# Kernel tuning notes

Measured on AMD Instinct MI355X. Metric: run time of the kernel, lower is better.

The kernel has to match this reference:

```python
import jax, jax.numpy as jnp
import numpy as np

MASK_FILL = jnp.float32(-2**32 + 1)

def dice(x, alpha):
    # x: (S, B, F); batch-dim (dim=0) mean/std, unbiased std like torch.std
    avg = x.mean(axis=0)
    std = jnp.std(x, axis=0, ddof=1)
    p = jax.nn.sigmoid((x - avg) / std)
    return x * p + alpha * x * (1.0 - p)

def setup_inputs() -> dict:
    key = jax.random.key(0)
    ks = jax.random.split(key, 12)
    S, B, D = 200, 1024, 128          # seq_len, batch, 2H
    F = 4 * D                          # num_features = 512
    L1, L2 = 80, 40
    inp = {
        "query": jax.random.normal(ks[0], (B, D), jnp.float32),
        "facts": jax.random.normal(ks[1], (S, B, D), jnp.float32),
        "mask": jax.random.randint(ks[2], (S, B), 0, 2).astype(bool),
        "W1": jax.random.normal(ks[3], (F, L1), jnp.float32) / np.sqrt(F),
        "b1": jnp.zeros((L1,), jnp.float32),
        "a1": jnp.zeros((1,), jnp.float32),
        "W2": jax.random.normal(ks[4], (L1, L2), jnp.float32) / np.sqrt(L1),
        "b2": jnp.zeros((L2,), jnp.float32),
        "a2": jnp.zeros((1,), jnp.float32),
        "W3": jax.random.normal(ks[5], (L2, 1), jnp.float32) / np.sqrt(L2),
        "b3": jnp.zeros((1,), jnp.float32),
    }
    return inp

def reference(query, facts, mask, W1, b1, a1, W2, b2, a2, W3, b3):
    S, B, D = facts.shape
    # faithful to torch: tile along feature dim then reshape (permutes elements)
    q2 = jnp.tile(query, (1, S)).reshape(S, B, D)
    x = jnp.concatenate([q2, facts, q2 * facts, q2 - facts], axis=-1)  # (S,B,4D)
    h = dice(jnp.einsum('sbf,fl->sbl', x, W1) + b1, a1)
    h = dice(jnp.einsum('sbf,fl->sbl', h, W2) + b2, a2)
    logits = (jnp.einsum('sbf,fl->sbl', h, W3) + b3).squeeze(-1)  # (S,B)
    masked = jnp.where(mask, logits, MASK_FILL)
    normalized = jax.nn.softmax(masked, axis=0)
    return normalized[..., None] * facts  # (S,B,D)
```

## Files before the change

kernel.cpp:

```cpp
#include <hip/hip_runtime.h>
#include <hip/hip_bf16.h>
#include <math.h>

#define SS 200
#define BB 1024
#define DD 128
#define FF 512
#define LL1 80
#define LL2 40
#define PP (SS*BB)
#define MASK_FILL_F (-4294967295.0f)
#define NTILE 13

typedef short bf16x8 __attribute__((ext_vector_type(8)));
typedef float f32x4  __attribute__((ext_vector_type(4)));

static __device__ __forceinline__ unsigned short f2bf(float x) {
    __hip_bfloat16 h = __float2bfloat16(x);
    return *reinterpret_cast<unsigned short*>(&h);
}
static __device__ __forceinline__ float bf2f(unsigned short u) {
    __hip_bfloat16 h = *reinterpret_cast<__hip_bfloat16*>(&u);
    return __bfloat162float(h);
}
static __device__ __forceinline__ void split8(const float* x, bf16x8& ah, bf16x8& al) {
#pragma unroll
    for (int j = 0; j < 8; ++j) {
        unsigned u = __float_as_uint(x[j]);
        ah[j] = (short)(u >> 16);
        float hi = __uint_as_float(u & 0xffff0000u);
        al[j] = (short)f2bf(x[j] - hi);
    }
}
static __device__ __forceinline__ float fast_sigmoid(float t) {
    return __builtin_amdgcn_rcpf(1.f + __expf(-t));
}

__global__ void k_prep_all(const float* __restrict__ W1, const float* __restrict__ W2,
                           const unsigned char* __restrict__ mask,
                           unsigned short* __restrict__ bfr1,
                           unsigned short* __restrict__ bfr2, int* __restrict__ flag) {
    const int blk = blockIdx.x;
    if (blk == 35) {
        if (threadIdx.x < 64) {
            const uchar4 u = ((const uchar4*)mask)[threadIdx.x];
            const bool f = ((u.y | u.z) | u.w) != 0;
            const unsigned long long anyf = __ballot(f);
            if (threadIdx.x == 0) *flag = (anyf != 0ull) ? 1 : 0;
        }
        return;
    }
    if (blk < 30) {
        int t = blk * 256 + threadIdx.x;
        if (t >= 120 * 64) return;
        int lane = t & 63;
        int fid  = t >> 6;
        int nt   = fid % 5;
        int hl   = (fid / 5) % 2;
        int step = (fid / 10) % 6;
        int h    = fid / 60;
        int ktL  = step / 3;
        int seg  = step - 3 * ktL;
        int kt   = h * 2 + ktL;
        int n     = nt * 16 + (lane & 15);
        int kbase = kt * 32 + (lane >> 4) * 8;
        unsigned short* o = bfr1 + (size_t)t * 8;
#pragma unroll
        for (int j = 0; j < 8; ++j) {
            int k = kbase + j;
            float w;
            if (seg == 0)      w = W1[k * LL1 + n] + W1[(384 + k) * LL1 + n];
            else if (seg == 1) w = W1[(128 + k) * LL1 + n] - W1[(384 + k) * LL1 + n];
            else               w = W1[(256 + k) * LL1 + n];
            unsigned short hb = f2bf(w);
            o[j] = (hl == 0) ? hb : f2bf(w - bf2f(hb));
        }
    } else {
        int t = (blk - 30) * 256 + threadIdx.x;
        if (t >= 18 * 64) return;
        int lane = t & 63;
        int fid  = t >> 6;
        int hl   = fid & 1;
        int nt   = (fid >> 1) % 3;
        int kt   = fid / 6;
        int n  = nt * 16 + (lane & 15);
        int kb = kt * 32 + (lane >> 4) * 8;
        unsigned short* o = bfr2 + (size_t)t * 8;
#pragma unroll
        for (int j = 0; j < 8; ++j) {
            int k = kb + j;
            float w = (k < LL1 && n < LL2) ? W2[k * LL2 + n] : 0.f;
            unsigned short hb = f2bf(w);
            o[j] = (hl == 0) ? hb : f2bf(w - bf2f(hb));
        }
    }
}

__global__ __launch_bounds__(512, 4) void k_fused(
    const float* __restrict__ query, const float* __restrict__ facts,
    const unsigned short* __restrict__ bfr1, const unsigned short* __restrict__ bfr2,
    const float* __restrict__ b1, const float* __restrict__ a1,
    const float* __restrict__ b2, const float* __restrict__ a2,
    const float* __restrict__ W3, const float* __restrict__ b3,
    const void* __restrict__ mask, const int* __restrict__ flag,
    float* __restrict__ wbufT) {
    const int tid  = threadIdx.x;
    const int w    = tid >> 6;
    const int lane = tid & 63;
    const int m    = lane & 15;
    const int quad = lane >> 4;
    const int b    = blockIdx.x;

    __shared__ __align__(16) float z1f[NTILE * 16 * 81 + 16];
    __shared__ float psum[480], pssq[480];
    __shared__ float smean[LL1], sistd[LL1];
    __shared__ float sw3[LL2];
    __shared__ float red[8];

    int tile[2], pr[2], qr[2];
    bool tl[2];
#pragma unroll
    for (int t = 0; t < 2; ++t) {
        tile[t] = t * 8 + w;
        tl[t]   = (tile[t] < NTILE);
        int s = tile[t] * 16 + m;
        if (s > SS - 1) s = SS - 1;
        pr[t] = s * BB + b;
        qr[t] = pr[t] / SS;
    }

    f32x4 acc[2][5];
#pragma unroll
    for (int t = 0; t < 2; ++t)
#pragma unroll
        for (int nt = 0; nt < 5; ++nt) acc[t][nt] = (f32x4){0.f, 0.f, 0.f, 0.f};

#pragma unroll 1
    for (int h = 0; h < 2; ++h) {
        if (h) __syncthreads();
        {
            const int4* src = (const int4*)bfr1 + h * 3840;
            int4* dst = (int4*)z1f;
#pragma unroll
            for (int it = 0; it < 8; ++it) {
                int idx = it * 512 + tid;
                if (idx < 3840) dst[idx] = src[idx];
            }
        }
        __syncthreads();
        const unsigned short* lbuf = (const unsigned short*)z1f;
#pragma unroll
        for (int ktL = 0; ktL < 2; ++ktL) {
            const int dbase = (h * 2 + ktL) * 32 + quad * 8;
            float q8[2][8], f8[2][8];
#pragma unroll
            for (int t = 0; t < 2; ++t) {
                if (!tl[t]) continue;
                const float* qp = query + (size_t)qr[t] * DD + dbase;
                const float* fp = facts + (size_t)pr[t] * DD + dbase;
                *(float4*)&q8[t][0] = *(const float4*)qp;
                *(float4*)&q8[t][4] = *(const float4*)(qp + 4);
                *(float4*)&f8[t][0] = *(const float4*)fp;
                *(float4*)&f8[t][4] = *(const float4*)(fp + 4);
            }
#pragma unroll
            for (int seg = 0; seg < 3; ++seg) {
                const int step = ktL * 3 + seg;
                bf16x8 Bh[5], Bl[5];
#pragma unroll
                for (int nt = 0; nt < 5; ++nt) {
                    Bh[nt] = *(const bf16x8*)&lbuf[((step * 2 + 0) * 5 + nt) * 512 + lane * 8];
                    Bl[nt] = *(const bf16x8*)&lbuf[((step * 2 + 1) * 5 + nt) * 512 + lane * 8];
                }
#pragma unroll
                for (int t = 0; t < 2; ++t) {
                    if (!tl[t]) continue;
                    float x8[8];
#pragma unroll
                    for (int j = 0; j < 8; ++j)
                        x8[j] = (seg == 0) ? q8[t][j]
                              : (seg == 1 ? f8[t][j] : q8[t][j] * f8[t][j]);
                    bf16x8 ah, al;
                    split8(x8, ah, al);
#pragma unroll
                    for (int nt = 0; nt < 5; ++nt) {
                        acc[t][nt] = __builtin_amdgcn_mfma_f32_16x16x32_bf16(ah, Bh[nt], acc[t][nt], 0, 0, 0);
                        acc[t][nt] = __builtin_amdgcn_mfma_f32_16x16x32_bf16(al, Bh[nt], acc[t][nt], 0, 0, 0);
                        acc[t][nt] = __builtin_amdgcn_mfma_f32_16x16x32_bf16(ah, Bl[nt], acc[t][nt], 0, 0, 0);
                    }
                }
            }
        }
    }

    __syncthreads();
    {
        float b1v[5];
#pragma unroll
        for (int nt = 0; nt < 5; ++nt) b1v[nt] = b1[nt * 16 + m];
#pragma unroll
        for (int t = 0; t < 2; ++t) {
            if (!tl[t]) continue;
#pragma unroll
            for (int nt = 0; nt < 5; ++nt)
#pragma unroll
                for (int r = 0; r < 4; ++r)
                    z1f[(tile[t] * 16 + quad * 4 + r) * 81 + nt * 16 + m] = acc[t][nt][r] + b1v[nt];
        }
    }
    __syncthreads();

    if (tid < 480) {
        const int l = tid % LL1, c = tid / LL1;
        const int s0 = c * 34;
        const int s1 = (s0 + 34 < SS) ? s0 + 34 : SS;
        float sum = 0.f, ssq = 0.f;
        for (int s = s0; s < s1; ++s) {
            float v = z1f[s * 81 + l];
            sum += v;
            ssq = fmaf(v, v, ssq);
        }
        psum[c * LL1 + l] = sum;
        pssq[c * LL1 + l] = ssq;
    }
    __syncthreads();
    if (tid < LL1) {
        float sum = 0.f, ssq = 0.f;
#pragma unroll
        for (int c = 0; c < 6; ++c) {
            sum += psum[c * LL1 + tid];
            ssq += pssq[c * LL1 + tid];
        }
        float mn  = sum * (1.f / SS);
        float var = (ssq - (float)SS * mn * mn) * (1.f / (SS - 1));
        smean[tid] = mn;
        sistd[tid] = rsqrtf(var);
    }
    __syncthreads();

    const float alpha1 = *a1;
    f32x4 acc2[2][3];
#pragma unroll
    for (int t = 0; t < 2; ++t)
#pragma unroll
        for (int nt = 0; nt < 3; ++nt) acc2[t][nt] = (f32x4){0.f, 0.f, 0.f, 0.f};

#pragma unroll
    for (int kt = 0; kt < 3; ++kt) {
        bf16x8 Bh[3], Bl[3];
#pragma unroll
        for (int nt = 0; nt < 3; ++nt) {
            Bh[nt] = *(const bf16x8*)(bfr2 + (size_t)((kt * 3 + nt) * 2 + 0) * 512 + lane * 8);
            Bl[nt] = *(const bf16x8*)(bfr2 + (size_t)((kt * 3 + nt) * 2 + 1) * 512 + lane * 8);
        }
        const int kb = kt * 32 + quad * 8;
        const bool lv = (kt < 2 || quad < 2);
#pragma unroll
        for (int t = 0; t < 2; ++t) {
            if (!tl[t]) continue;
            float x8[8];
            if (lv) {
                const float* zr = &z1f[(tile[t] * 16 + m) * 81 + kb];
#pragma unroll
                for (int j = 0; j < 8; ++j) {
                    float v  = zr[j];
                    float pp = fast_sigmoid((v - smean[kb + j]) * sistd[kb + j]);
                    x8[j] = v * (alpha1 + (1.f - alpha1) * pp);
                }
            } else {
#pragma unroll
                for (int j = 0; j < 8; ++j) x8[j] = 0.f;
            }
            bf16x8 ah, al;
            split8(x8, ah, al);
#pragma unroll
            for (int nt = 0; nt < 3; ++nt) {
                acc2[t][nt] = __builtin_amdgcn_mfma_f32_16x16x32_bf16(ah, Bh[nt], acc2[t][nt], 0, 0, 0);
                acc2[t][nt] = __builtin_amdgcn_mfma_f32_16x16x32_bf16(al, Bh[nt], acc2[t][nt], 0, 0, 0);
                acc2[t][nt] = __builtin_amdgcn_mfma_f32_16x16x32_bf16(ah, Bl[nt], acc2[t][nt], 0, 0, 0);
            }
        }
    }
    __syncthreads();

    {
        float b2v[3];
#pragma unroll
        for (int nt = 0; nt < 3; ++nt) {
            const int n = nt * 16 + m;
            b2v[nt] = (n < LL2) ? b2[n] : 0.f;
        }
#pragma unroll
        for (int t = 0; t < 2; ++t) {
            if (!tl[t]) continue;
#pragma unroll
            for (int r = 0; r < 4; ++r) {
                const int srow = tile[t] * 16 + quad * 4 + r;
                if (srow >= SS) continue;
#pragma unroll
                for (int nt = 0; nt < 3; ++nt) {
                    const int n = nt * 16 + m;
                    if (n < LL2) z1f[srow * 41 + n] = acc2[t][nt][r] + b2v[nt];
                }
            }
        }
    }
    __syncthreads();

    if (tid < 480) {
        const int l = tid % LL2, c = tid / LL2;
        const int s0 = c * 17;
        const int s1 = (s0 + 17 < SS) ? s0 + 17 : SS;
        float sum = 0.f, ssq = 0.f;
        for (int s = s0; s < s1; ++s) {
            float v = z1f[s * 41 + l];
            sum += v;
            ssq = fmaf(v, v, ssq);
        }
        psum[c * LL2 + l] = sum;
        pssq[c * LL2 + l] = ssq;
    }
    __syncthreads();
    if (tid < LL2) {
        float sum = 0.f, ssq = 0.f;
#pragma unroll
        for (int c = 0; c < 12; ++c) {
            sum += psum[c * LL2 + tid];
            ssq += pssq[c * LL2 + tid];
        }
        float mn  = sum * (1.f / SS);
        float var = (ssq - (float)SS * mn * mn) * (1.f / (SS - 1));
        smean[tid] = mn;
        sistd[tid] = rsqrtf(var);
        sw3[tid]   = W3[tid];
    }
    __syncthreads();

    const float alpha2 = *a2;
    const int boolLayout = *flag;
    float logit = -3.0e38f;
    if (tid < SS) {
        float dot = b3[0];
#pragma unroll
        for (int k = 0; k < LL2; ++k) {
            float v  = z1f[tid * 41 + k];
            float pp = fast_sigmoid((v - smean[k]) * sistd[k]);
            float hh = v * (pp + alpha2 * (1.f - pp));
            dot = fmaf(hh, sw3[k], dot);
        }
        const int mi = tid * BB + b;
        const bool mk = boolLayout ? (((const unsigned char*)mask)[mi] != 0)
                                   : (((const int*)mask)[mi] != 0);
        logit = mk ? dot : MASK_FILL_F;
    }
    float v = logit;
#pragma unroll
    for (int off = 1; off < 64; off <<= 1) v = fmaxf(v, __shfl_xor(v, off, 64));
    if ((tid & 63) == 0) red[tid >> 6] = v;
    __syncthreads();
    float smax = red[0];
#pragma unroll
    for (int i = 1; i < 8; ++i) smax = fmaxf(smax, red[i]);
    __syncthreads();
    const float e = (tid < SS) ? __expf(logit - smax) : 0.f;
    v = e;
#pragma unroll
    for (int off = 1; off < 64; off <<= 1) v += __shfl_xor(v, off, 64);
    if ((tid & 63) == 0) red[tid >> 6] = v;
    __syncthreads();
    float ssum = red[0];
#pragma unroll
    for (int i = 1; i < 8; ++i) ssum += red[i];
    const float inv = __builtin_amdgcn_rcpf(ssum);
    if (tid < SS) wbufT[(size_t)b * SS + tid] = e * inv;
}

__global__ __launch_bounds__(256) void k4_scale(
    const float* __restrict__ wbufT, const float* __restrict__ facts,
    float* __restrict__ out) {
    int i = blockIdx.x * 256 + threadIdx.x;
    int p = i >> 5;
    float w = wbufT[(size_t)(p & (BB - 1)) * SS + (p >> 10)];
    float4 f = ((const float4*)facts)[i];
    float4 o;
    o.x = f.x * w; o.y = f.y * w; o.z = f.z * w; o.w = f.w * w;
    ((float4*)out)[i] = o;
}

extern "C" void kernel_launch(void* const* d_in, const int* in_sizes, int n_in,
                              void* d_out, int out_size, void* d_ws, size_t ws_size,
                              hipStream_t stream) {
    const float* query = (const float*)d_in[0];
    const float* facts = (const float*)d_in[1];
    const void*  mask  = d_in[2];
    const float* W1 = (const float*)d_in[3];
    const float* b1 = (const float*)d_in[4];
    const float* a1 = (const float*)d_in[5];
    const float* W2 = (const float*)d_in[6];
    const float* b2 = (const float*)d_in[7];
    const float* a2 = (const float*)d_in[8];
    const float* W3 = (const float*)d_in[9];
    const float* b3 = (const float*)d_in[10];
    float* out = (float*)d_out;

    unsigned short* bfr1 = (unsigned short*)(out + 24739840);
    unsigned short* bfr2 = (unsigned short*)(out + 24801280);
    float* wbufT = (float*)d_ws;
    int*   flag  = (int*)((char*)d_ws + 900 * 1024);

    k_prep_all<<<36, 256, 0, stream>>>(W1, W2, (const unsigned char*)mask, bfr1, bfr2, flag);
    k_fused<<<BB, 512, 0, stream>>>(query, facts, bfr1, bfr2, b1, a1, b2, a2,
                                    W3, b3, mask, flag, wbufT);
    k4_scale<<<(PP * DD) / (256 * 4), 256, 0, stream>>>(wbufT, facts, out);
}
```

Baseline: 328.9 us.

## Split fused kernel into a coalesced MFMA layer-1 kernel and per-batch reduction kernel

The fused per-batch kernel loaded facts and query rows strided across the sequence dimension, one batch column per block. The first-layer MFMA GEMM now runs in its own kernel over contiguous position tiles, giving coalesced facts reads and more blocks. It writes the pre-activation z1 transposed, in batch-major order, into the output buffer as scratch. A second kernel then reloads each batch's z1 slab for the Dice statistics, layer 2 and the softmax. This adds a round trip of about 65 MB through global memory plus an extra launch.

```diff
diff --git a/kernel.cpp b/kernel.cpp
--- a/kernel.cpp
+++ b/kernel.cpp
@@ -96,14 +96,103 @@
     }
 }
 
-__global__ __launch_bounds__(512, 4) void k_fused(
+__global__ __launch_bounds__(256, 4) void k1_mfma(
     const float* __restrict__ query, const float* __restrict__ facts,
-    const unsigned short* __restrict__ bfr1, const unsigned short* __restrict__ bfr2,
-    const float* __restrict__ b1, const float* __restrict__ a1,
-    const float* __restrict__ b2, const float* __restrict__ a2,
-    const float* __restrict__ W3, const float* __restrict__ b3,
-    const void* __restrict__ mask, const int* __restrict__ flag,
-    float* __restrict__ wbufT) {
+    const unsigned short* __restrict__ bfr, const float* __restrict__ b1,
+    float* __restrict__ z1T) {
+    const int tid  = threadIdx.x;
+    const int lane = tid & 63;
+    const int m    = lane & 15;
+    const int quad = lane >> 4;
+    const int pw   = blockIdx.x * 128 + (tid >> 6) * 32;
+
+    __shared__ __align__(16) unsigned short lbuf[15360];
+
+    f32x4 acc[2][5];
+#pragma unroll
+    for (int t = 0; t < 2; ++t)
+#pragma unroll
+        for (int nt = 0; nt < 5; ++nt) acc[t][nt] = (f32x4){0.f, 0.f, 0.f, 0.f};
+
+    int pr[2], qr[2];
+#pragma unroll
+    for (int t = 0; t < 2; ++t) {
+        pr[t] = pw + t * 16 + m;
+        qr[t] = pr[t] / SS;
+    }
+
+#pragma unroll 1
+    for (int kt = 0; kt < 4; ++kt) {
+        const int dbase = kt * 32 + quad * 8;
+        float q8[2][8], f8[2][8];
+#pragma unroll
+        for (int t = 0; t < 2; ++t) {
+            const float* qp = query + (size_t)qr[t] * DD + dbase;
+            const float* fp = facts + (size_t)pr[t] * DD + dbase;
+            *(float4*)&q8[t][0] = *(const float4*)qp;
+            *(float4*)&q8[t][4] = *(const float4*)(qp + 4);
+            *(float4*)&f8[t][0] = *(const float4*)fp;
+            *(float4*)&f8[t][4] = *(const float4*)(fp + 4);
+        }
+        if (kt) __syncthreads();
+        {
+            const int4* src = (const int4*)bfr + kt * 1920;
+#pragma unroll
+            for (int it = 0; it < 8; ++it) {
+                int idx = it * 256 + tid;
+                if (idx < 1920) ((int4*)lbuf)[idx] = src[idx];
+            }
+        }
+        __syncthreads();
+
+#pragma unroll
+        for (int seg = 0; seg < 3; ++seg) {
+            bf16x8 Bh[5], Bl[5];
+#pragma unroll
+            for (int nt = 0; nt < 5; ++nt) {
+                Bh[nt] = *(const bf16x8*)&lbuf[((seg * 2 + 0) * 5 + nt) * 512 + lane * 8];
+                Bl[nt] = *(const bf16x8*)&lbuf[((seg * 2 + 1) * 5 + nt) * 512 + lane * 8];
+            }
+#pragma unroll
+            for (int t = 0; t < 2; ++t) {
+                float x8[8];
+#pragma unroll
+                for (int j = 0; j < 8; ++j)
+                    x8[j] = (seg == 0) ? q8[t][j]
+                          : (seg == 1 ? f8[t][j] : q8[t][j] * f8[t][j]);
+                bf16x8 ah, al;
+                split8(x8, ah, al);
+#pragma unroll
+                for (int nt = 0; nt < 5; ++nt) {
+                    acc[t][nt] = __builtin_amdgcn_mfma_f32_16x16x32_bf16(ah, Bh[nt], acc[t][nt], 0, 0, 0);
+                    acc[t][nt] = __builtin_amdgcn_mfma_f32_16x16x32_bf16(al, Bh[nt], acc[t][nt], 0, 0, 0);
+                    acc[t][nt] = __builtin_amdgcn_mfma_f32_16x16x32_bf16(ah, Bl[nt], acc[t][nt], 0, 0, 0);
+                }
+            }
+        }
+    }
+#pragma unroll
+    for (int t = 0; t < 2; ++t)
+#pragma unroll
+        for (int nt = 0; nt < 5; ++nt) {
+            const int n = nt * 16 + m;
+            const float bias = b1[n];
+#pragma unroll
+            for (int r = 0; r < 4; ++r) {
+                const int p = pw + t * 16 + quad * 4 + r;
+                const int s = p >> 10;
+                const int b = p & (BB - 1);
+                z1T[((size_t)b * SS + s) * LL1 + n] = acc[t][nt][r] + bias;
+            }
+        }
+}
+
+__global__ __launch_bounds__(512, 2) void k_light(
+    const float* __restrict__ z1T, const unsigned short* __restrict__ bfr2,
+    const float* __restrict__ a1, const float* __restrict__ b2,
+    const float* __restrict__ a2, const float* __restrict__ W3,
+    const float* __restrict__ b3, const void* __restrict__ mask,
+    const int* __restrict__ flag, float* __restrict__ wbufT) {
     const int tid  = threadIdx.x;
     const int w    = tid >> 6;
     const int lane = tid & 63;
@@ -111,102 +200,22 @@
     const int quad = lane >> 4;
     const int b    = blockIdx.x;
 
-    __shared__ __align__(16) float z1f[NTILE * 16 * 81 + 16];
+    __shared__ __align__(16) float z1f[NTILE * 16 * 81 + 8];
     __shared__ float psum[480], pssq[480];
     __shared__ float smean[LL1], sistd[LL1];
     __shared__ float sw3[LL2];
     __shared__ float red[8];
 
-    int tile[2], pr[2], qr[2];
-    bool tl[2];
-#pragma unroll
-    for (int t = 0; t < 2; ++t) {
-        tile[t] = t * 8 + w;
-        tl[t]   = (tile[t] < NTILE);
-        int s = tile[t] * 16 + m;
-        if (s > SS - 1) s = SS - 1;
-        pr[t] = s * BB + b;
-        qr[t] = pr[t] / SS;
-    }
-
-    f32x4 acc[2][5];
-#pragma unroll
-    for (int t = 0; t < 2; ++t)
-#pragma unroll
-        for (int nt = 0; nt < 5; ++nt) acc[t][nt] = (f32x4){0.f, 0.f, 0.f, 0.f};
-
-#pragma unroll 1
-    for (int h = 0; h < 2; ++h) {
-        if (h) __syncthreads();
-        {
-            const int4* src = (const int4*)bfr1 + h * 3840;
-            int4* dst = (int4*)z1f;
-#pragma unroll
-            for (int it = 0; it < 8; ++it) {
-                int idx = it * 512 + tid;
-                if (idx < 3840) dst[idx] = src[idx];
-            }
-        }
-        __syncthreads();
-        const unsigned short* lbuf = (const unsigned short*)z1f;
-#pragma unroll
-        for (int ktL = 0; ktL < 2; ++ktL) {
-            const int dbase = (h * 2 + ktL) * 32 + quad * 8;
-            float q8[2][8], f8[2][8];
-#pragma unroll
-            for (int t = 0; t < 2; ++t) {
-                if (!tl[t]) continue;
-                const float* qp = query + (size_t)qr[t] * DD + dbase;
-                const float* fp = facts + (size_t)pr[t] * DD + dbase;
-                *(float4*)&q8[t][0] = *(const float4*)qp;
-                *(float4*)&q8[t][4] = *(const float4*)(qp + 4);
-                *(float4*)&f8[t][0] = *(const float4*)fp;
-                *(float4*)&f8[t][4] = *(const float4*)(fp + 4);
-            }
-#pragma unroll
-            for (int seg = 0; seg < 3; ++seg) {
-                const int step = ktL * 3 + seg;
-                bf16x8 Bh[5], Bl[5];
-#pragma unroll
-                for (int nt = 0; nt < 5; ++nt) {
-                    Bh[nt] = *(const bf16x8*)&lbuf[((step * 2 + 0) * 5 + nt) * 512 + lane * 8];
-                    Bl[nt] = *(const bf16x8*)&lbuf[((step * 2 + 1) * 5 + nt) * 512 + lane * 8];
-                }
-#pragma unroll
-                for (int t = 0; t < 2; ++t) {
-                    if (!tl[t]) continue;
-                    float x8[8];
-#pragma unroll
-                    for (int j = 0; j < 8; ++j)
-                        x8[j] = (seg == 0) ? q8[t][j]
-                              : (seg == 1 ? f8[t][j] : q8[t][j] * f8[t][j]);
-                    bf16x8 ah, al;
-                    split8(x8, ah, al);
-#pragma unroll
-                    for (int nt = 0; nt < 5; ++nt) {
-                        acc[t][nt] = __builtin_amdgcn_mfma_f32_16x16x32_bf16(ah, Bh[nt], acc[t][nt], 0, 0, 0);
-                        acc[t][nt] = __builtin_amdgcn_mfma_f32_16x16x32_bf16(al, Bh[nt], acc[t][nt], 0, 0, 0);
-                        acc[t][nt] = __builtin_amdgcn_mfma_f32_16x16x32_bf16(ah, Bl[nt], acc[t][nt], 0, 0, 0);
-                    }
-                }
-            }
-        }
-    }
-
-    __syncthreads();
     {
-        float b1v[5];
-#pragma unroll
-        for (int nt = 0; nt < 5; ++nt) b1v[nt] = b1[nt * 16 + m];
-#pragma unroll
-        for (int t = 0; t < 2; ++t) {
-            if (!tl[t]) continue;
-#pragma unroll
-            for (int nt = 0; nt < 5; ++nt)
-#pragma unroll
-                for (int r = 0; r < 4; ++r)
-                    z1f[(tile[t] * 16 + quad * 4 + r) * 81 + nt * 16 + m] = acc[t][nt][r] + b1v[nt];
-        }
+        const float4* src = (const float4*)(z1T + (size_t)b * (SS * LL1));
+        for (int i = tid; i < (SS * LL1) / 4; i += 512) {
+            float4 v = src[i];
+            int s = i / 20;
+            int o = (i - s * 20) * 4;
+            float* d = &z1f[s * 81 + o];
+            d[0] = v.x; d[1] = v.y; d[2] = v.z; d[3] = v.w;
+        }
+        for (int i = tid; i < 8 * 81; i += 512) z1f[SS * 81 + i] = 0.f;
     }
     __syncthreads();
 
@@ -244,6 +253,14 @@
     for (int t = 0; t < 2; ++t)
 #pragma unroll
         for (int nt = 0; nt < 3; ++nt) acc2[t][nt] = (f32x4){0.f, 0.f, 0.f, 0.f};
+
+    int tile[2];
+    bool tl[2];
+#pragma unroll
+    for (int t = 0; t < 2; ++t) {
+        tile[t] = t * 8 + w;
+        tl[t]   = (tile[t] < NTILE);
+    }
 
 #pragma unroll
     for (int kt = 0; kt < 3; ++kt) {
@@ -403,13 +420,14 @@
     const float* b3 = (const float*)d_in[10];
     float* out = (float*)d_out;
 
+    float* z1T = out;
     unsigned short* bfr1 = (unsigned short*)(out + 24739840);
     unsigned short* bfr2 = (unsigned short*)(out + 24801280);
     float* wbufT = (float*)d_ws;
     int*   flag  = (int*)((char*)d_ws + 900 * 1024);
 
     k_prep_all<<<36, 256, 0, stream>>>(W1, W2, (const unsigned char*)mask, bfr1, bfr2, flag);
-    k_fused<<<BB, 512, 0, stream>>>(query, facts, bfr1, bfr2, b1, a1, b2, a2,
-                                    W3, b3, mask, flag, wbufT);
+    k1_mfma<<<PP / 128, 256, 0, stream>>>(query, facts, bfr1, b1, z1T);
+    k_light<<<BB, 512, 0, stream>>>(z1T, bfr2, a1, b2, a2, W3, b3, mask, flag, wbufT);
     k4_scale<<<(PP * DD) / (256 * 4), 256, 0, stream>>>(wbufT, facts, out);
 }
```

After: 368.5 us. 12.0% more time.
